# Kernel tuning notes

Hardware: AMD Instinct MI355X
Metric: run time of the kernel (lower is better)

## Reference

```python
import jax, jax.numpy as jnp
import numpy as np

B, S, DM, H, D = 2, 1024, 1024, 16, 64  # batch, seq, d_model, heads, head_dim


def setup_inputs() -> dict:
    key = jax.random.key(0)
    ks = jax.random.split(key, 16)
    sc = 1.0 / np.sqrt(DM)
    scd = 1.0 / np.sqrt(D)
    return {
        "hidden_states": jax.random.normal(ks[0], (B, S, DM), dtype=jnp.float32),
        # frozen base_attn projections
        "Wq": jax.random.normal(ks[1], (DM, DM), dtype=jnp.float32) * sc,
        "bq": jnp.zeros((DM,), dtype=jnp.float32),
        "Wk": jax.random.normal(ks[2], (DM, DM), dtype=jnp.float32) * sc,
        "bk": jnp.zeros((DM,), dtype=jnp.float32),
        "Wv": jax.random.normal(ks[3], (DM, DM), dtype=jnp.float32) * sc,
        "bv": jnp.zeros((DM,), dtype=jnp.float32),
        "Wo": jax.random.normal(ks[4], (DM, DM), dtype=jnp.float32) * sc,
        "bo": jnp.zeros((DM,), dtype=jnp.float32),
        # trainable hedgehog feature maps (per-head Linear(head_dim, head_dim))
        "Wfq": jax.random.normal(ks[5], (D, D), dtype=jnp.float32) * scd,
        "bfq": jnp.zeros((D,), dtype=jnp.float32),
        "Wfk": jax.random.normal(ks[6], (D, D), dtype=jnp.float32) * scd,
        "bfk": jnp.zeros((D,), dtype=jnp.float32),
    }


def _heads(x):
    # (B, S, DM) -> (B, H, S, D)
    return x.reshape(B, S, H, D).transpose(0, 2, 1, 3)


def _feature_map(x, W, b):
    # HedgehogFeatureMap: Linear then concat(exp(x), exp(-x)) along last dim
    y = jnp.einsum('bhsd,ed->bhse', x, W) + b
    return jnp.concatenate([jnp.exp(y), jnp.exp(-y)], axis=-1)  # (B,H,S,2D)


def reference(hidden_states, Wq, bq, Wk, bk, Wv, bv, Wo, bo, Wfq, bfq, Wfk, bfk):
    # base_attn: standard multi-head softmax attention with output_attentions=True
    q = _heads(hidden_states @ Wq.T + bq)
    k = _heads(hidden_states @ Wk.T + bk)
    v = _heads(hidden_states @ Wv.T + bv)
    scores = jnp.einsum('bhmd,bhnd->bhmn', q, k) / jnp.sqrt(jnp.float32(D))
    true_attns = jax.nn.softmax(scores, axis=-1)  # (B,H,S,S)
    ctx = jnp.einsum('bhmn,bhnd->bhmd', true_attns, v)
    outputs = ctx.transpose(0, 2, 1, 3).reshape(B, S, DM) @ Wo.T + bo

    # hedgehog path: feature maps on q/k then sum-normalized quadratic attention
    fq = _feature_map(q, Wfq, bfq)
    fk = _feature_map(k, Wfk, bfk)
    qk = jnp.einsum('bhmd,bhnd->bhmn', fq, fk)
    pred_attns = qk / jnp.sum(qk, axis=-1, keepdims=True)
    return (outputs, pred_attns, true_attns)
```

## Files before the change

### kernel.cpp

```cpp
#include <hip/hip_runtime.h>
#include <math.h>

constexpr int B_ = 2, S_ = 1024, DM_ = 1024, NH_ = 16, HD_ = 64;
constexpr long SD = (long)S_ * DM_;
constexpr long SS = (long)S_ * S_;

typedef _Float16 half8 __attribute__((ext_vector_type(8)));
typedef _Float16 half4 __attribute__((ext_vector_type(4)));
typedef float floatx4 __attribute__((ext_vector_type(4)));

__device__ __forceinline__ void gl_lds16(const void* g, void* l) {
    __builtin_amdgcn_global_load_lds(
        (const __attribute__((address_space(1))) void*)g,
        (__attribute__((address_space(3))) void*)l, 16, 0, 0);
}

__global__ __launch_bounds__(256) void cvt_f2h(
    const float* __restrict__ x, _Float16* __restrict__ y, int n4)
{
    int i = (blockIdx.x * 256 + threadIdx.x);
    if (i < n4) {
        float4 v = ((const float4*)x)[i];
        half4 h = { (_Float16)v.x, (_Float16)v.y, (_Float16)v.z, (_Float16)v.w };
        ((half4*)y)[i] = h;
    }
}

template <int BM, int BN, int WM, int WN, int CONVA>
__global__ __launch_bounds__(256) void mm_nt(
    const void* __restrict__ Ap, const _Float16* __restrict__ Wp,
    const float* __restrict__ bias, float* __restrict__ Cf,
    _Float16* __restrict__ Ch, int K, int lda, int ldw, int ldc,
    long sAb, long sAh, long sWb, long sWh, long sCb, long sCh,
    float scale, int mode)
{
    constexpr int MI = WM / 16, NI = WN / 16;
    const int z = blockIdx.z, b = z / NH_, h = z % NH_;
    const int wave = threadIdx.x >> 6, lane = threadIdx.x & 63;
    const int m0 = blockIdx.y * BM, n0 = blockIdx.x * BN;
    const int wm = (wave >> 1) * WM, wn = (wave & 1) * WN;
    const int r16 = lane & 15, quad = lane >> 4;

    const _Float16* Wz = Wp + (long)b * sWb + (long)h * sWh;

    __shared__ __align__(16) _Float16 As[BM * 32];
    __shared__ __align__(16) _Float16 Bs[BN * 32];

    floatx4 acc[MI][NI];
#pragma unroll
    for (int i = 0; i < MI; ++i)
#pragma unroll
        for (int j = 0; j < NI; ++j)
#pragma unroll
            for (int r = 0; r < 4; ++r) acc[i][j][r] = 0.f;

    for (int k0 = 0; k0 < K; k0 += 32) {
        if constexpr (CONVA) {
            const float* Af = (const float*)Ap + (long)b * sAb + (long)h * sAh;
#pragma unroll
            for (int r = 0; r < BM / 32; ++r) {
                int idx = r * 1024 + threadIdx.x * 4;
                int row = idx >> 5, col = idx & 31;
                float4 v = *(const float4*)(Af + (long)(m0 + row) * lda + k0 + col);
                half4 hv = { (_Float16)v.x, (_Float16)v.y, (_Float16)v.z, (_Float16)v.w };
                *(half4*)&As[row * 32 + col] = hv;
            }
        } else {
            const _Float16* Ah = (const _Float16*)Ap + (long)b * sAb + (long)h * sAh;
#pragma unroll
            for (int c = wave * (BM / 64); c < (wave + 1) * (BM / 64); ++c) {
                const _Float16* g = Ah + (long)(m0 + c * 16 + (lane >> 2)) * lda
                                    + k0 + (lane & 3) * 8;
                gl_lds16(g, &As[c * 512]);
            }
        }
#pragma unroll
        for (int c = wave * (BN / 64); c < (wave + 1) * (BN / 64); ++c) {
            const _Float16* g = Wz + (long)(n0 + c * 16 + (lane >> 2)) * ldw
                                + k0 + (lane & 3) * 8;
            gl_lds16(g, &Bs[c * 512]);
        }
        __syncthreads();

        half8 af[MI], bf8[NI];
#pragma unroll
        for (int i = 0; i < MI; ++i)
            af[i] = *(const half8*)&As[(wm + i * 16 + r16) * 32 + quad * 8];
#pragma unroll
        for (int j = 0; j < NI; ++j)
            bf8[j] = *(const half8*)&Bs[(wn + j * 16 + r16) * 32 + quad * 8];
#pragma unroll
        for (int i = 0; i < MI; ++i)
#pragma unroll
            for (int j = 0; j < NI; ++j)
                acc[i][j] = __builtin_amdgcn_mfma_f32_16x16x32_f16(
                    af[i], bf8[j], acc[i][j], 0, 0, 0);
        __syncthreads();
    }

    const long cb = (long)b * sCb + (long)h * sCh;
#pragma unroll
    for (int i = 0; i < MI; ++i) {
#pragma unroll
        for (int j = 0; j < NI; ++j) {
#pragma unroll
            for (int r = 0; r < 4; ++r) {
                int row = m0 + wm + i * 16 + quad * 4 + r;
                int col = n0 + wn + j * 16 + r16;
                float v = acc[i][j][r] * scale;
                if (bias) v += bias[col];
                if (mode == 0) Cf[cb + (long)row * ldc + col] = v;
                else           Ch[cb + (long)row * ldc + col] = (_Float16)v;
            }
        }
    }
}

__global__ __launch_bounds__(256) void qkv_proj(
    const _Float16* __restrict__ hsH,
    const _Float16* __restrict__ W0, const _Float16* __restrict__ W1,
    const _Float16* __restrict__ W2,
    const float* __restrict__ b0, const float* __restrict__ b1,
    const float* __restrict__ b2,
    _Float16* __restrict__ QH, _Float16* __restrict__ KH,
    _Float16* __restrict__ VtH)
{
    const int z = blockIdx.z;
    const _Float16* W = (z == 0) ? W0 : (z == 1) ? W1 : W2;
    const float* bias = (z == 0) ? b0 : (z == 1) ? b1 : b2;

    const int wave = threadIdx.x >> 6, lane = threadIdx.x & 63;
    const int m0 = blockIdx.y * 128, n0 = blockIdx.x * 128;
    const int wm = (wave >> 1) * 64, wn = (wave & 1) * 64;
    const int r16 = lane & 15, quad = lane >> 4;

    __shared__ __align__(16) _Float16 As[128 * 32];
    __shared__ __align__(16) _Float16 Bs[128 * 32];

    floatx4 acc[4][4];
#pragma unroll
    for (int i = 0; i < 4; ++i)
#pragma unroll
        for (int j = 0; j < 4; ++j)
#pragma unroll
            for (int r = 0; r < 4; ++r) acc[i][j][r] = 0.f;

    for (int k0 = 0; k0 < 1024; k0 += 32) {
#pragma unroll
        for (int c = wave * 2; c < wave * 2 + 2; ++c) {
            const _Float16* ga = hsH + (long)(m0 + c * 16 + (lane >> 2)) * 1024
                                 + k0 + (lane & 3) * 8;
            gl_lds16(ga, &As[c * 512]);
            const _Float16* gb = W + (long)(n0 + c * 16 + (lane >> 2)) * 1024
                                 + k0 + (lane & 3) * 8;
            gl_lds16(gb, &Bs[c * 512]);
        }
        __syncthreads();

        half8 af[4], bf8[4];
#pragma unroll
        for (int i = 0; i < 4; ++i)
            af[i] = *(const half8*)&As[(wm + i * 16 + r16) * 32 + quad * 8];
#pragma unroll
        for (int j = 0; j < 4; ++j)
            bf8[j] = *(const half8*)&Bs[(wn + j * 16 + r16) * 32 + quad * 8];
#pragma unroll
        for (int i = 0; i < 4; ++i)
#pragma unroll
            for (int j = 0; j < 4; ++j)
                acc[i][j] = __builtin_amdgcn_mfma_f32_16x16x32_f16(
                    af[i], bf8[j], acc[i][j], 0, 0, 0);
        __syncthreads();
    }

    _Float16* dst = (z == 0) ? QH : KH;
#pragma unroll
    for (int i = 0; i < 4; ++i) {
#pragma unroll
        for (int j = 0; j < 4; ++j) {
#pragma unroll
            for (int r = 0; r < 4; ++r) {
                int row = m0 + wm + i * 16 + quad * 4 + r;
                int col = n0 + wn + j * 16 + r16;
                float v = acc[i][j][r] + bias[col];
                if (z < 2) {
                    dst[(long)row * 1024 + col] = (_Float16)v;
                } else {
                    int bb = row >> 10, s = row & 1023;
                    int hh = col >> 6, d = col & 63;
                    VtH[((((long)bb * 16 + hh) * 64 + d) << 10) | s] = (_Float16)v;
                }
            }
        }
    }
}

__global__ __launch_bounds__(256) void feat_map(
    const _Float16* __restrict__ Xh, const _Float16* __restrict__ Wf,
    const float* __restrict__ bf, _Float16* __restrict__ outH)
{
    const int z = blockIdx.y, b = z >> 4, h = z & 15;
    const int m0 = blockIdx.x * 64;
    __shared__ float Xs[64][65];
    __shared__ float Ws[64][65];
    const _Float16* Xb = Xh + (long)b * SD + h * 64;
    for (int i = threadIdx.x; i < 4096; i += 256) {
        int r = i >> 6, c = i & 63;
        Xs[r][c] = (float)Xb[(long)(m0 + r) * 1024 + c];
        Ws[r][c] = (float)Wf[i];
    }
    __syncthreads();
    const int tm = (threadIdx.x >> 4) * 4, tn = (threadIdx.x & 15) * 4;
    float acc[4][4] = {{0.f}};
    for (int k = 0; k < 64; ++k) {
        float xv[4], wv[4];
#pragma unroll
        for (int i = 0; i < 4; ++i) xv[i] = Xs[tm + i][k];
#pragma unroll
        for (int j = 0; j < 4; ++j) wv[j] = Ws[tn + j][k];
#pragma unroll
        for (int i = 0; i < 4; ++i)
#pragma unroll
            for (int j = 0; j < 4; ++j) acc[i][j] = fmaf(xv[i], wv[j], acc[i][j]);
    }
#pragma unroll
    for (int i = 0; i < 4; ++i) {
        long base = ((long)z * S_ + m0 + tm + i) * 128;
#pragma unroll
        for (int j = 0; j < 4; ++j) {
            float y = acc[i][j] + bf[tn + j];
            outH[base + tn + j]      = (_Float16)expf(y);
            outH[base + 64 + tn + j] = (_Float16)expf(-y);
        }
    }
}

__global__ __launch_bounds__(256) void softmax_rows(float* __restrict__ data)
{
    const long row = blockIdx.x;
    float* p = data + row * (long)S_;
    const int t = threadIdx.x;
    float x[4];
#pragma unroll
    for (int i = 0; i < 4; ++i) x[i] = p[t + i * 256];

    float m = fmaxf(fmaxf(x[0], x[1]), fmaxf(x[2], x[3]));
#pragma unroll
    for (int o = 32; o > 0; o >>= 1) m = fmaxf(m, __shfl_down(m, o, 64));
    __shared__ float sm[4];
    if ((t & 63) == 0) sm[t >> 6] = m;
    __syncthreads();
    m = fmaxf(fmaxf(sm[0], sm[1]), fmaxf(sm[2], sm[3]));

    float s = 0.f;
#pragma unroll
    for (int i = 0; i < 4; ++i) { x[i] = expf(x[i] - m); s += x[i]; }
#pragma unroll
    for (int o = 32; o > 0; o >>= 1) s += __shfl_down(s, o, 64);
    __shared__ float ss[4];
    if ((t & 63) == 0) ss[t >> 6] = s;
    __syncthreads();
    s = ss[0] + ss[1] + ss[2] + ss[3];

    float inv = 1.f / s;
#pragma unroll
    for (int i = 0; i < 4; ++i) p[t + i * 256] = x[i] * inv;
}

__global__ __launch_bounds__(256) void norm_rows(float* __restrict__ data)
{
    const long row = blockIdx.x;
    float* p = data + row * (long)S_;
    const int t = threadIdx.x;
    float x[4];
#pragma unroll
    for (int i = 0; i < 4; ++i) x[i] = p[t + i * 256];

    float s = x[0] + x[1] + x[2] + x[3];
#pragma unroll
    for (int o = 32; o > 0; o >>= 1) s += __shfl_down(s, o, 64);
    __shared__ float ss[4];
    if ((t & 63) == 0) ss[t >> 6] = s;
    __syncthreads();
    s = ss[0] + ss[1] + ss[2] + ss[3];

    float inv = 1.f / s;
#pragma unroll
    for (int i = 0; i < 4; ++i) p[t + i * 256] = x[i] * inv;
}

extern "C" void kernel_launch(void* const* d_in, const int* in_sizes, int n_in,
                              void* d_out, int out_size, void* d_ws, size_t ws_size,
                              hipStream_t stream)
{
    (void)in_sizes; (void)n_in; (void)out_size; (void)ws_size;

    const float* hs  = (const float*)d_in[0];
    const float* Wq  = (const float*)d_in[1];
    const float* bq  = (const float*)d_in[2];
    const float* Wk  = (const float*)d_in[3];
    const float* bk  = (const float*)d_in[4];
    const float* Wv  = (const float*)d_in[5];
    const float* bv  = (const float*)d_in[6];
    const float* Wo  = (const float*)d_in[7];
    const float* bo  = (const float*)d_in[8];
    const float* Wfq = (const float*)d_in[9];
    const float* bfq = (const float*)d_in[10];
    const float* Wfk = (const float*)d_in[11];
    const float* bfk = (const float*)d_in[12];

    float* out0  = (float*)d_out;
    float* pred  = out0 + (long)B_ * S_ * DM_;
    float* trueA = pred + (long)B_ * NH_ * S_ * S_;

    _Float16* hsH  = (_Float16*)d_ws;
    _Float16* WqH  = hsH + 2 * 1024 * 1024;
    _Float16* WkH  = WqH + 1024 * 1024;
    _Float16* WvH  = WkH + 1024 * 1024;
    _Float16* WoH  = WvH + 1024 * 1024;
    _Float16* WfqH = WoH + 1024 * 1024;
    _Float16* WfkH = WfqH + 4096;
    _Float16* QH   = WfkH + 4096;
    _Float16* KH   = QH + 2 * 1024 * 1024;
    _Float16* VtH  = KH + 2 * 1024 * 1024;
    _Float16* ctxH = VtH + 2 * 1024 * 1024;
    _Float16* fqH  = ctxH + 2 * 1024 * 1024;
    _Float16* fkH  = fqH + (long)B_ * NH_ * S_ * 128;

    const dim3 blk(256);

    cvt_f2h<<<2048, blk, 0, stream>>>(hs, hsH, 512 * 1024);
    cvt_f2h<<<1024, blk, 0, stream>>>(Wq, WqH, 256 * 1024);
    cvt_f2h<<<1024, blk, 0, stream>>>(Wk, WkH, 256 * 1024);
    cvt_f2h<<<1024, blk, 0, stream>>>(Wv, WvH, 256 * 1024);
    cvt_f2h<<<1024, blk, 0, stream>>>(Wo, WoH, 256 * 1024);
    cvt_f2h<<<4, blk, 0, stream>>>(Wfq, WfqH, 1024);
    cvt_f2h<<<4, blk, 0, stream>>>(Wfk, WfkH, 1024);

    qkv_proj<<<dim3(8, 16, 3), blk, 0, stream>>>(
        hsH, WqH, WkH, WvH, bq, bk, bv, QH, KH, VtH);

    mm_nt<128, 128, 64, 64, 0><<<dim3(8, 8, 32), blk, 0, stream>>>(
        QH, KH, nullptr, trueA, nullptr, 64, 1024, 1024, 1024,
        SD, 64, SD, 64, 16 * SS, SS, 0.125f, 0);

    softmax_rows<<<B_ * NH_ * S_, blk, 0, stream>>>(trueA);

    mm_nt<128, 64, 64, 32, 1><<<dim3(1, 8, 32), blk, 0, stream>>>(
        trueA, VtH, nullptr, nullptr, ctxH, 1024, 1024, 1024, 1024,
        16 * SS, SS, (long)16 * 64 * 1024, (long)64 * 1024, SD, 64, 1.f, 1);

    mm_nt<128, 128, 64, 64, 0><<<dim3(8, 16, 1), blk, 0, stream>>>(
        ctxH, WoH, bo, out0, nullptr, 1024, 1024, 1024, 1024,
        0, 0, 0, 0, 0, 0, 1.f, 0);

    feat_map<<<dim3(16, 32), blk, 0, stream>>>(QH, WfqH, bfq, fqH);
    feat_map<<<dim3(16, 32), blk, 0, stream>>>(KH, WfkH, bfk, fkH);

    mm_nt<128, 128, 64, 64, 0><<<dim3(8, 8, 32), blk, 0, stream>>>(
        fqH, fkH, nullptr, pred, nullptr, 128, 128, 128, 1024,
        (long)16 * S_ * 128, (long)S_ * 128,
        (long)16 * S_ * 128, (long)S_ * 128,
        16 * SS, SS, 1.f, 0);

    norm_rows<<<B_ * NH_ * S_, blk, 0, stream>>>(pred);
}
```

Baseline: 539.6 us.

## Fuse QK, softmax and PV into one attention kernel; fold hedgehog normalization into GEMM

Replaces the separate QK^T GEMM, row softmax pass and PV GEMM with one kernel. Each 512-thread block computes a 32-row score tile over all 1024 keys, does the softmax in registers, writes the fp32 probabilities once, and keeps an fp16 copy in LDS for the PV product. This removes the round trips that re-read the two 128 MB score tensors. The hedgehog row sums are now computed algebraically as fq·sum(fk), and the scaling is applied in the GEMM epilogue, which drops the norm_rows pass. The Wo projection tile is also changed to 64x128. The cost is a 64 KB LDS buffer and reduced occupancy in the fused kernel, plus scratch space reused from the converted Wq buffer.

```diff
diff --git a/kernel.cpp b/kernel.cpp
--- a/kernel.cpp
+++ b/kernel.cpp
@@ -29,7 +29,8 @@
 template <int BM, int BN, int WM, int WN, int CONVA>
 __global__ __launch_bounds__(256) void mm_nt(
     const void* __restrict__ Ap, const _Float16* __restrict__ Wp,
-    const float* __restrict__ bias, float* __restrict__ Cf,
+    const float* __restrict__ bias, const float* __restrict__ rowscale,
+    float* __restrict__ Cf,
     _Float16* __restrict__ Ch, int K, int lda, int ldw, int ldc,
     long sAb, long sAh, long sWb, long sWh, long sCb, long sCh,
     float scale, int mode)
@@ -109,6 +110,7 @@
                 int col = n0 + wn + j * 16 + r16;
                 float v = acc[i][j][r] * scale;
                 if (bias) v += bias[col];
+                if (rowscale) v *= rowscale[(long)z * 1024 + row];
                 if (mode == 0) Cf[cb + (long)row * ldc + col] = v;
                 else           Ch[cb + (long)row * ldc + col] = (_Float16)v;
             }
@@ -195,6 +197,181 @@
     }
 }
 
+__global__ __launch_bounds__(512) void attn_fused(
+    const _Float16* __restrict__ Q, const _Float16* __restrict__ K,
+    const _Float16* __restrict__ Vt, float* __restrict__ trueA,
+    _Float16* __restrict__ ctx)
+{
+    const int z = blockIdx.y, b = z >> 4, h = z & 15;
+    const int m0 = blockIdx.x * 32;
+    const int wave = threadIdx.x >> 6, lane = threadIdx.x & 63;
+    const int r16 = lane & 15, quad = lane >> 4;
+    const int c0 = wave * 128;
+
+    __shared__ __align__(16) _Float16 Ps[32 * 1024];
+    float* redmx = (float*)Ps;
+    float* redsm = (float*)Ps + 256;
+    float* kred  = (float*)Ps;
+
+    const _Float16* Qb = Q + (long)b * SD + h * 64;
+    const _Float16* Kb = K + (long)b * SD + h * 64;
+
+    half8 af[2][2];
+#pragma unroll
+    for (int mi = 0; mi < 2; ++mi)
+#pragma unroll
+        for (int ks = 0; ks < 2; ++ks)
+            af[mi][ks] = *(const half8*)&Qb[(long)(m0 + mi * 16 + r16) * DM_
+                                            + ks * 32 + quad * 8];
+
+    floatx4 acc[2][8];
+#pragma unroll
+    for (int mi = 0; mi < 2; ++mi)
+#pragma unroll
+        for (int nj = 0; nj < 8; ++nj)
+#pragma unroll
+            for (int r = 0; r < 4; ++r) acc[mi][nj][r] = 0.f;
+
+#pragma unroll
+    for (int ks = 0; ks < 2; ++ks) {
+#pragma unroll
+        for (int nj = 0; nj < 8; ++nj) {
+            half8 bf = *(const half8*)&Kb[(long)(c0 + nj * 16 + r16) * DM_
+                                          + ks * 32 + quad * 8];
+            acc[0][nj] = __builtin_amdgcn_mfma_f32_16x16x32_f16(
+                af[0][ks], bf, acc[0][nj], 0, 0, 0);
+            acc[1][nj] = __builtin_amdgcn_mfma_f32_16x16x32_f16(
+                af[1][ks], bf, acc[1][nj], 0, 0, 0);
+        }
+    }
+
+    float rmx[2][4];
+#pragma unroll
+    for (int mi = 0; mi < 2; ++mi)
+#pragma unroll
+        for (int r = 0; r < 4; ++r) {
+            float m = acc[mi][0][r];
+#pragma unroll
+            for (int nj = 1; nj < 8; ++nj) m = fmaxf(m, acc[mi][nj][r]);
+#pragma unroll
+            for (int o = 1; o <= 8; o <<= 1) m = fmaxf(m, __shfl_xor(m, o, 64));
+            rmx[mi][r] = m;
+        }
+    if (r16 == 0) {
+#pragma unroll
+        for (int mi = 0; mi < 2; ++mi)
+#pragma unroll
+            for (int r = 0; r < 4; ++r)
+                redmx[wave * 32 + mi * 16 + quad * 4 + r] = rmx[mi][r];
+    }
+    __syncthreads();
+    float mx[2][4];
+#pragma unroll
+    for (int mi = 0; mi < 2; ++mi)
+#pragma unroll
+        for (int r = 0; r < 4; ++r) {
+            float m = redmx[mi * 16 + quad * 4 + r];
+#pragma unroll
+            for (int w = 1; w < 8; ++w)
+                m = fmaxf(m, redmx[w * 32 + mi * 16 + quad * 4 + r]);
+            mx[mi][r] = m;
+        }
+
+    float rsm[2][4];
+#pragma unroll
+    for (int mi = 0; mi < 2; ++mi)
+#pragma unroll
+        for (int r = 0; r < 4; ++r) {
+            float s = 0.f;
+#pragma unroll
+            for (int nj = 0; nj < 8; ++nj) {
+                float p = __expf((acc[mi][nj][r] - mx[mi][r]) * 0.125f);
+                acc[mi][nj][r] = p;
+                s += p;
+            }
+#pragma unroll
+            for (int o = 1; o <= 8; o <<= 1) s += __shfl_xor(s, o, 64);
+            rsm[mi][r] = s;
+        }
+    if (r16 == 0) {
+#pragma unroll
+        for (int mi = 0; mi < 2; ++mi)
+#pragma unroll
+            for (int r = 0; r < 4; ++r)
+                redsm[wave * 32 + mi * 16 + quad * 4 + r] = rsm[mi][r];
+    }
+    __syncthreads();
+    float inv[2][4];
+#pragma unroll
+    for (int mi = 0; mi < 2; ++mi)
+#pragma unroll
+        for (int r = 0; r < 4; ++r) {
+            float s = 0.f;
+#pragma unroll
+            for (int w = 0; w < 8; ++w)
+                s += redsm[w * 32 + mi * 16 + quad * 4 + r];
+            inv[mi][r] = 1.f / s;
+        }
+    __syncthreads();
+
+    float* Ta = trueA + (long)z * SS + (long)m0 * S_;
+#pragma unroll
+    for (int mi = 0; mi < 2; ++mi) {
+#pragma unroll
+        for (int r = 0; r < 4; ++r) {
+            const int row = mi * 16 + quad * 4 + r;
+            const int sw = (row & 7) << 3;
+            const float iv = inv[mi][r];
+#pragma unroll
+            for (int nj = 0; nj < 8; ++nj) {
+                const int col = c0 + nj * 16 + r16;
+                const float v = acc[mi][nj][r] * iv;
+                Ta[(long)row * S_ + col] = v;
+                Ps[row * 1024 + (col ^ sw)] = (_Float16)v;
+            }
+        }
+    }
+    __syncthreads();
+
+    const int d0 = (wave & 3) * 16, kr = wave >> 2;
+    const _Float16* Vb = Vt + ((long)z * 64 + d0 + r16) * (long)S_;
+    floatx4 c2[2];
+#pragma unroll
+    for (int mi = 0; mi < 2; ++mi)
+#pragma unroll
+        for (int r = 0; r < 4; ++r) c2[mi][r] = 0.f;
+
+    const int swz = (r16 & 7) << 3;
+#pragma unroll 4
+    for (int k0 = kr * 512; k0 < kr * 512 + 512; k0 += 32) {
+        half8 pa0 = *(const half8*)&Ps[r16 * 1024 + ((k0 + quad * 8) ^ swz)];
+        half8 pa1 = *(const half8*)&Ps[(16 + r16) * 1024 + ((k0 + quad * 8) ^ swz)];
+        half8 vf  = *(const half8*)&Vb[k0 + quad * 8];
+        c2[0] = __builtin_amdgcn_mfma_f32_16x16x32_f16(pa0, vf, c2[0], 0, 0, 0);
+        c2[1] = __builtin_amdgcn_mfma_f32_16x16x32_f16(pa1, vf, c2[1], 0, 0, 0);
+    }
+
+    __syncthreads();
+    if (kr == 1) {
+#pragma unroll
+        for (int mi = 0; mi < 2; ++mi)
+            *(floatx4*)&kred[(((wave & 3) * 2 + mi) * 64 + lane) * 4] = c2[mi];
+    }
+    __syncthreads();
+    if (kr == 0) {
+        _Float16* Cb = ctx + (long)b * SD + h * 64;
+#pragma unroll
+        for (int mi = 0; mi < 2; ++mi) {
+            c2[mi] += *(const floatx4*)&kred[((wave * 2 + mi) * 64 + lane) * 4];
+#pragma unroll
+            for (int r = 0; r < 4; ++r) {
+                const int srow = m0 + mi * 16 + quad * 4 + r;
+                Cb[(long)srow * DM_ + d0 + r16] = (_Float16)c2[mi][r];
+            }
+        }
+    }
+}
+
 __global__ __launch_bounds__(256) void feat_map(
     const _Float16* __restrict__ Xh, const _Float16* __restrict__ Wf,
     const float* __restrict__ bf, _Float16* __restrict__ outH)
@@ -235,58 +412,37 @@
     }
 }
 
-__global__ __launch_bounds__(256) void softmax_rows(float* __restrict__ data)
-{
-    const long row = blockIdx.x;
-    float* p = data + row * (long)S_;
-    const int t = threadIdx.x;
-    float x[4];
-#pragma unroll
-    for (int i = 0; i < 4; ++i) x[i] = p[t + i * 256];
-
-    float m = fmaxf(fmaxf(x[0], x[1]), fmaxf(x[2], x[3]));
-#pragma unroll
-    for (int o = 32; o > 0; o >>= 1) m = fmaxf(m, __shfl_down(m, o, 64));
-    __shared__ float sm[4];
-    if ((t & 63) == 0) sm[t >> 6] = m;
-    __syncthreads();
-    m = fmaxf(fmaxf(sm[0], sm[1]), fmaxf(sm[2], sm[3]));
-
+__global__ __launch_bounds__(256) void sum_fk(
+    const _Float16* __restrict__ fkH, float* __restrict__ sk)
+{
+    const int z = blockIdx.x;
+    const int col = threadIdx.x & 127, hlf = threadIdx.x >> 7;
+    const _Float16* p = fkH + (long)z * S_ * 128 + (long)hlf * 512 * 128 + col;
     float s = 0.f;
-#pragma unroll
-    for (int i = 0; i < 4; ++i) { x[i] = expf(x[i] - m); s += x[i]; }
-#pragma unroll
-    for (int o = 32; o > 0; o >>= 1) s += __shfl_down(s, o, 64);
-    __shared__ float ss[4];
-    if ((t & 63) == 0) ss[t >> 6] = s;
-    __syncthreads();
-    s = ss[0] + ss[1] + ss[2] + ss[3];
-
-    float inv = 1.f / s;
-#pragma unroll
-    for (int i = 0; i < 4; ++i) p[t + i * 256] = x[i] * inv;
-}
-
-__global__ __launch_bounds__(256) void norm_rows(float* __restrict__ data)
-{
-    const long row = blockIdx.x;
-    float* p = data + row * (long)S_;
-    const int t = threadIdx.x;
-    float x[4];
-#pragma unroll
-    for (int i = 0; i < 4; ++i) x[i] = p[t + i * 256];
-
-    float s = x[0] + x[1] + x[2] + x[3];
-#pragma unroll
-    for (int o = 32; o > 0; o >>= 1) s += __shfl_down(s, o, 64);
-    __shared__ float ss[4];
-    if ((t & 63) == 0) ss[t >> 6] = s;
-    __syncthreads();
-    s = ss[0] + ss[1] + ss[2] + ss[3];
-
-    float inv = 1.f / s;
-#pragma unroll
-    for (int i = 0; i < 4; ++i) p[t + i * 256] = x[i] * inv;
+    for (int i = 0; i < 512; ++i) s += (float)p[(long)i * 128];
+    __shared__ float part[2][128];
+    part[hlf][col] = s;
+    __syncthreads();
+    if (threadIdx.x < 128)
+        sk[z * 128 + threadIdx.x] = part[0][threadIdx.x] + part[1][threadIdx.x];
+}
+
+__global__ __launch_bounds__(256) void rowsum_inv(
+    const _Float16* __restrict__ fqH, const float* __restrict__ sk,
+    float* __restrict__ rsinv)
+{
+    const int g = blockIdx.x * 256 + threadIdx.x;
+    const int z = g >> 10;
+    const _Float16* p = fqH + (long)g * 128;
+    const float* s = sk + z * 128;
+    float acc = 0.f;
+#pragma unroll
+    for (int d0 = 0; d0 < 128; d0 += 8) {
+        half8 v = *(const half8*)(p + d0);
+#pragma unroll
+        for (int j = 0; j < 8; ++j) acc = fmaf((float)v[j], s[d0 + j], acc);
+    }
+    rsinv[g] = 1.f / acc;
 }
 
 extern "C" void kernel_launch(void* const* d_in, const int* in_sizes, int n_in,
@@ -327,6 +483,9 @@
     _Float16* fqH  = ctxH + 2 * 1024 * 1024;
     _Float16* fkH  = fqH + (long)B_ * NH_ * S_ * 128;
 
+    float* sk    = (float*)WqH;
+    float* rsinv = sk + 32 * 128;
+
     const dim3 blk(256);
 
     cvt_f2h<<<2048, blk, 0, stream>>>(hs, hsH, 512 * 1024);
@@ -340,28 +499,22 @@
     qkv_proj<<<dim3(8, 16, 3), blk, 0, stream>>>(
         hsH, WqH, WkH, WvH, bq, bk, bv, QH, KH, VtH);
 
-    mm_nt<128, 128, 64, 64, 0><<<dim3(8, 8, 32), blk, 0, stream>>>(
-        QH, KH, nullptr, trueA, nullptr, 64, 1024, 1024, 1024,
-        SD, 64, SD, 64, 16 * SS, SS, 0.125f, 0);
-
-    softmax_rows<<<B_ * NH_ * S_, blk, 0, stream>>>(trueA);
-
-    mm_nt<128, 64, 64, 32, 1><<<dim3(1, 8, 32), blk, 0, stream>>>(
-        trueA, VtH, nullptr, nullptr, ctxH, 1024, 1024, 1024, 1024,
-        16 * SS, SS, (long)16 * 64 * 1024, (long)64 * 1024, SD, 64, 1.f, 1);
-
-    mm_nt<128, 128, 64, 64, 0><<<dim3(8, 16, 1), blk, 0, stream>>>(
-        ctxH, WoH, bo, out0, nullptr, 1024, 1024, 1024, 1024,
+    attn_fused<<<dim3(32, 32), dim3(512), 0, stream>>>(
+        QH, KH, VtH, trueA, ctxH);
+
+    mm_nt<64, 128, 32, 64, 0><<<dim3(8, 32, 1), blk, 0, stream>>>(
+        ctxH, WoH, bo, nullptr, out0, nullptr, 1024, 1024, 1024, 1024,
         0, 0, 0, 0, 0, 0, 1.f, 0);
 
     feat_map<<<dim3(16, 32), blk, 0, stream>>>(QH, WfqH, bfq, fqH);
     feat_map<<<dim3(16, 32), blk, 0, stream>>>(KH, WfkH, bfk, fkH);
 
+    sum_fk<<<32, blk, 0, stream>>>(fkH, sk);
+    rowsum_inv<<<128, blk, 0, stream>>>(fqH, sk, rsinv);
+
     mm_nt<128, 128, 64, 64, 0><<<dim3(8, 8, 32), blk, 0, stream>>>(
-        fqH, fkH, nullptr, pred, nullptr, 128, 128, 128, 1024,
+        fqH, fkH, nullptr, rsinv, pred, nullptr, 128, 128, 128, 1024,
         (long)16 * S_ * 128, (long)S_ * 128,
         (long)16 * S_ * 128, (long)S_ * 128,
         16 * SS, SS, 1.f, 0);
-
-    norm_rows<<<B_ * NH_ * S_, blk, 0, stream>>>(pred);
-}
+}
```

Result: faster. 486.4 us (-9.9%).
